# Kernel tuning notes

Measured on AMD Instinct MI355X. Metric: run time of the kernel, lower is better.

The kernel has to match this reference:

```python
import jax, jax.numpy as jnp
import numpy as np
import math

D_MODEL = 1024
NHEAD = 16
D_K = D_MODEL // NHEAD
LAMDA_ATT = 1.0
B, L = 2, 2048


def setup_inputs() -> dict:
    key = jax.random.key(0)
    ks = jax.random.split(key, 10)
    s = 1.0 / math.sqrt(D_MODEL)
    x = jax.random.normal(ks[0], (B, L, D_MODEL), dtype=jnp.float32)
    delta_r = jax.random.uniform(ks[1], (B, L), dtype=jnp.float32)  # positive, fed to log
    Wq = jax.random.normal(ks[2], (D_MODEL, D_MODEL), dtype=jnp.float32) * s
    Wk = jax.random.normal(ks[3], (D_MODEL, D_MODEL), dtype=jnp.float32) * s
    Wv = jax.random.normal(ks[4], (D_MODEL, D_MODEL), dtype=jnp.float32) * s
    Wo = jax.random.normal(ks[5], (D_MODEL, D_MODEL), dtype=jnp.float32) * s
    bq = jnp.zeros((D_MODEL,), jnp.float32)
    bk = jnp.zeros((D_MODEL,), jnp.float32)
    bv = jnp.zeros((D_MODEL,), jnp.float32)
    bo = jnp.zeros((D_MODEL,), jnp.float32)
    return {"x": x, "delta_r": delta_r, "Wq": Wq, "bq": bq, "Wk": Wk, "bk": bk,
            "Wv": Wv, "bv": bv, "Wo": Wo, "bo": bo}


def reference(x, delta_r, Wq, bq, Wk, bk, Wv, bv, Wo, bo):
    b, l, d = x.shape
    h, dk = NHEAD, D_K

    def proj(y, W, bias):
        # [B,L,D] -> [B,H,L,dk]
        return (y @ W + bias).reshape(b, l, h, dk).transpose(0, 2, 1, 3)

    v_scaled = x * delta_r[..., None]
    q = proj(x, Wq, bq)
    k = proj(x, Wk, bk)
    v = proj(v_scaled, Wv, bv)

    scores = jnp.einsum('bhqd,bhkd->bhqk', q, k) / math.sqrt(dk)
    pos = jnp.arange(l)
    dist = jnp.abs(pos[None, :] - pos[:, None]).astype(scores.dtype)  # [L,L]
    rel_bias = LAMDA_ATT * jnp.log(delta_r + 1e-6)  # [B,L]
    scores = scores - dist[None, None] * 0.1 + rel_bias[:, None, None, :]

    attn = jax.nn.softmax(scores, axis=-1)  # dropout is identity in eval mode
    context = jnp.einsum('bhqk,bhkd->bqhd', attn, v).reshape(b, l, d)
    out = context @ Wo + bo
    return out, attn.mean(axis=1)
```

## Files before the change

kernel.cpp:

```cpp
#include <hip/hip_runtime.h>
#include <math.h>

#define DMODEL 1024
#define NHEAD  16
#define DK     64
#define BB     2
#define LL     2048
#define MTOT   (BB*LL)

#define LOG2E      1.4426950408889634f
#define SCQ        (0.125f * LOG2E)
#define C2LOG      (0.1f * LOG2E)
#define SKIP_BOUND (-24.0f)

typedef __bf16 bf16_t;
typedef __bf16 bf16x8 __attribute__((ext_vector_type(8)));
typedef __bf16 bf16x4 __attribute__((ext_vector_type(4)));
typedef float  f32x4  __attribute__((ext_vector_type(4)));

static __device__ __forceinline__ f32x4 mfma16(bf16x8 a, bf16x8 b, f32x4 c) {
    return __builtin_amdgcn_mfma_f32_16x16x32_bf16(a, b, c, 0, 0, 0);
}
static __device__ __forceinline__ float exp2f_fast(float x) {
    return __builtin_amdgcn_exp2f(x);
}
static __device__ __forceinline__ float log2f_fast(float x) {
    return __builtin_amdgcn_logf(x);
}
static __device__ __forceinline__ void gl_lds16(const bf16_t* g, bf16_t* l) {
    __builtin_amdgcn_global_load_lds(
        (const __attribute__((address_space(1))) unsigned int*)g,
        (__attribute__((address_space(3))) unsigned int*)l, 16, 0, 0);
}

__global__ __launch_bounds__(256) void prep_x_k(
    const float* __restrict__ x, const float* __restrict__ dr,
    bf16_t* __restrict__ xb, float* __restrict__ logd2)
{
    size_t gid = (size_t)blockIdx.x * 256 + threadIdx.x;
    size_t off = gid * 8;
    float4 a = *(const float4*)(x + off);
    float4 c = *(const float4*)(x + off + 4);
    float va[8] = {a.x, a.y, a.z, a.w, c.x, c.y, c.z, c.w};
    bf16x8 o1;
#pragma unroll
    for (int j = 0; j < 8; ++j) o1[j] = (bf16_t)va[j];
    *(bf16x8*)(xb + off) = o1;
    if (gid < MTOT) logd2[gid] = log2f_fast(dr[gid] + 1e-6f);
}

__global__ __launch_bounds__(256) void prep_w_k(
    const float* __restrict__ Wq, const float* __restrict__ Wk,
    const float* __restrict__ Wv, const float* __restrict__ Wo,
    bf16_t* __restrict__ Wcat, bf16_t* __restrict__ Wot)
{
    __shared__ __align__(16) float Ts[64][68];
    const int z = blockIdx.z;
    const float* W = (z == 0) ? Wq : (z == 1) ? Wk : (z == 2) ? Wv : Wo;
    bf16_t* dst = (z < 3) ? (Wcat + (size_t)z * DMODEL * DMODEL) : Wot;
    const int tid = threadIdx.x;
    const int k0 = blockIdx.x * 64, n0 = blockIdx.y * 64;
#pragma unroll
    for (int i = 0; i < 4; ++i) {
        int u = tid + 256 * i, r = u >> 4, c4 = (u & 15) * 4;
        *(float4*)&Ts[r][c4] = *(const float4*)(W + (size_t)(k0 + r) * DMODEL + n0 + c4);
    }
    __syncthreads();
#pragma unroll
    for (int i = 0; i < 2; ++i) {
        int u = tid + 256 * i, n = u >> 3, k8 = (u & 7) * 8;
        bf16x8 v;
#pragma unroll
        for (int j = 0; j < 8; ++j) v[j] = (bf16_t)Ts[k8 + j][n];
        *(bf16x8*)(dst + (size_t)(n0 + n) * DMODEL + k0 + k8) = v;
    }
}

__global__ __launch_bounds__(256, 3) void gemm128_k(
    const bf16_t* __restrict__ A, const bf16_t* __restrict__ Bt,
    const float* __restrict__ b0, const float* __restrict__ b1,
    const float* __restrict__ b2, const float* __restrict__ delta,
    float* __restrict__ outf, bf16_t* __restrict__ outQ,
    bf16_t* __restrict__ outK, bf16_t* __restrict__ outVt, int mode)
{
    __shared__ __align__(16) bf16_t Asw[128 * 64];
    __shared__ __align__(16) bf16_t Bsw[128 * 64];
    const int tid = threadIdx.x, lane = tid & 63, w = tid >> 6;
    const int quad = lane >> 4, n16 = lane & 15;
    const int wm = (w & 1) * 64, wn = (w >> 1) * 64;
    const int m0 = blockIdx.y * 128, n0 = blockIdx.x * 128;
    const int srow = lane >> 3;
    const int scb  = (lane & 7) ^ srow;

    f32x4 acc[4][4] = {};

    for (int K0 = 0; K0 < DMODEL; K0 += 64) {
        __syncthreads();
#pragma unroll
        for (int i = 0; i < 4; ++i) {
            int rb = w * 32 + i * 8;
            gl_lds16(A  + (size_t)(m0 + rb + srow) * DMODEL + K0 + scb * 8,
                     &Asw[rb * 64]);
            gl_lds16(Bt + (size_t)(n0 + rb + srow) * DMODEL + K0 + scb * 8,
                     &Bsw[rb * 64]);
        }
        __syncthreads();
#pragma unroll
        for (int kc = 0; kc < 2; ++kc) {
            const int pcb = ((kc * 4 + quad) ^ (n16 & 7)) * 8;
            bf16x8 af[4], bfv[4];
#pragma unroll
            for (int mi = 0; mi < 4; ++mi)
                af[mi] = *(const bf16x8*)&Asw[(wm + mi * 16 + n16) * 64 + pcb];
#pragma unroll
            for (int ni = 0; ni < 4; ++ni)
                bfv[ni] = *(const bf16x8*)&Bsw[(wn + ni * 16 + n16) * 64 + pcb];
#pragma unroll
            for (int mi = 0; mi < 4; ++mi)
#pragma unroll
                for (int ni = 0; ni < 4; ++ni)
                    acc[mi][ni] = mfma16(af[mi], bfv[ni], acc[mi][ni]);
        }
    }

    if (mode == 0) {
        const int region = n0 >> 10;
        if (region == 2) {
#pragma unroll
            for (int mi = 0; mi < 4; ++mi) {
                const int mbase = m0 + wm + mi * 16 + quad * 4;
                const int bidx = mbase >> 11, l = mbase & (LL - 1);
                const f32x4 dm4 = *(const f32x4*)(delta + mbase);
#pragma unroll
                for (int ni = 0; ni < 4; ++ni) {
                    const int nl = (n0 & 1023) + wn + ni * 16 + n16;
                    const int h = nl >> 6, dd = nl & 63;
                    const float bv = b2[nl];
                    bf16x4 pk;
#pragma unroll
                    for (int r = 0; r < 4; ++r)
                        pk[r] = (bf16_t)(acc[mi][ni][r] * dm4[r] + bv);
                    *(bf16x4*)(outVt + ((size_t)(bidx * NHEAD + h) * DK + dd) * LL + l) = pk;
                }
            }
        } else {
            const float* bias = (region == 0) ? b0 : b1;
            bf16_t* dst = (region == 0) ? outQ : outK;
            const float qs = (region == 0) ? SCQ : 1.0f;
#pragma unroll
            for (int mi = 0; mi < 4; ++mi) {
#pragma unroll
                for (int r = 0; r < 4; ++r) {
                    const int m = m0 + wm + mi * 16 + quad * 4 + r;
                    const int bidx = m >> 11, l = m & (LL - 1);
#pragma unroll
                    for (int ni = 0; ni < 4; ++ni) {
                        const int nl = (n0 & 1023) + wn + ni * 16 + n16;
                        const int h = nl >> 6, dd = nl & 63;
                        float v = (acc[mi][ni][r] + bias[nl]) * qs;
                        dst[(((size_t)(bidx * NHEAD + h) * LL) + l) * DK + dd] = (bf16_t)v;
                    }
                }
            }
        }
    } else {
#pragma unroll
        for (int mi = 0; mi < 4; ++mi) {
#pragma unroll
            for (int r = 0; r < 4; ++r) {
                const int m = m0 + wm + mi * 16 + quad * 4 + r;
#pragma unroll
                for (int ni = 0; ni < 4; ++ni) {
                    const int n = n0 + wn + ni * 16 + n16;
                    outf[(size_t)m * DMODEL + n] = acc[mi][ni][r] + b0[n];
                }
            }
        }
    }
}

__global__ __launch_bounds__(256) void stats_k(
    const bf16_t* __restrict__ Q, const bf16_t* __restrict__ K,
    const float* __restrict__ logd2, float* __restrict__ Qn,
    float* __restrict__ Kn, float* __restrict__ dlb, float* __restrict__ ldx)
{
    __shared__ float qn_s[2048], kn_s[2048], dg_s[2048];
    const int tid = threadIdx.x, bh = blockIdx.x, b = bh >> 4;
    const size_t base = (size_t)bh * LL * DK;
#pragma unroll
    for (int i = 0; i < 8; ++i) {
        const int row = tid + 256 * i;
        float qn2 = 0.f, kn2 = 0.f, dg = 0.f;
#pragma unroll
        for (int j = 0; j < 8; ++j) {
            bf16x8 qv = *(const bf16x8*)(Q + base + (size_t)row * DK + j * 8);
            bf16x8 kv = *(const bf16x8*)(K + base + (size_t)row * DK + j * 8);
#pragma unroll
            for (int e = 0; e < 8; ++e) {
                float fq = (float)qv[e], fk = (float)kv[e];
                qn2 += fq * fq; kn2 += fk * fk; dg += fq * fk;
            }
        }
        qn_s[row] = qn2;
        kn_s[row] = kn2;
        dg_s[row] = dg + logd2[b * LL + row];
    }
    __syncthreads();
    if (tid < 16) {
        float mq = 0.f, md = 1e30f;
        for (int r = 0; r < 128; ++r) {
            mq = fmaxf(mq, qn_s[tid * 128 + r]);
            md = fminf(md, dg_s[tid * 128 + r]);
        }
        Qn[bh * 16 + tid] = sqrtf(mq);
        dlb[bh * 16 + tid] = md;
    } else if (tid >= 64 && tid < 96) {
        const int t = tid - 64;
        float mk = 0.f;
        for (int r = 0; r < 64; ++r) mk = fmaxf(mk, kn_s[t * 64 + r]);
        Kn[bh * 32 + t] = sqrtf(mk);
    } else if (tid >= 128 && tid < 160 && (bh & 15) == 0) {
        const int t = tid - 128;
        float ml = -1e30f;
        for (int r = 0; r < 64; ++r) ml = fmaxf(ml, logd2[b * LL + t * 64 + r]);
        ldx[b * 32 + t] = ml;
    }
}

__global__ __launch_bounds__(256) void mlstat_k(
    const float* __restrict__ mlws, float* __restrict__ mlmin)
{
    __shared__ float s[2048];
    const int tid = threadIdx.x, bh = blockIdx.x;
#pragma unroll
    for (int i = 0; i < 8; ++i)
        s[tid + 256 * i] = mlws[(size_t)bh * LL + tid + 256 * i];
    __syncthreads();
    if (tid < 16) {
        float m = 1e30f;
        for (int r = 0; r < 128; ++r) m = fminf(m, s[tid * 128 + r]);
        mlmin[bh * 16 + tid] = m;
    }
}

__global__ __launch_bounds__(256, 3) void attn_flash_mfma_k(
    const bf16_t* __restrict__ Q, const bf16_t* __restrict__ K,
    const bf16_t* __restrict__ Vt, const float* __restrict__ logd2,
    const float* __restrict__ Qn, const float* __restrict__ Kn,
    const float* __restrict__ dlb, const float* __restrict__ ldx,
    bf16_t* __restrict__ ctx, float* __restrict__ mlout)
{
    __shared__ __align__(16) bf16_t Ks[64][72];
    __shared__ __align__(16) bf16_t Vts[64][72];
    __shared__ __align__(16) bf16_t Ps[4][32][72];
    __shared__ float logds[64];

    const int tid = threadIdx.x;
    const int lane = tid & 63, w = tid >> 6;
    const int quad = lane >> 4, n16 = lane & 15;
    const int bh = blockIdx.x, b = bh >> 4, h = bh & 15;
    const int qt = blockIdx.y, q0 = qt * 128;
    const size_t base = (size_t)bh * LL * DK;
    const int qq[2] = {q0 + w * 32 + n16, q0 + w * 32 + 16 + n16};

    bf16x8 qa[2][2];
#pragma unroll
    for (int qg = 0; qg < 2; ++qg)
#pragma unroll
        for (int kc = 0; kc < 2; ++kc)
            qa[qg][kc] = *(const bf16x8*)(Q + base + (size_t)qq[qg] * DK +
                                          kc * 32 + quad * 8);

    unsigned mask = 0;
    {
        const float qn = Qn[bh * 16 + qt], dl = dlb[bh * 16 + qt];
        for (int t = 0; t < 32; ++t) {
            const int kc0 = t * 64;
            const int dmin = (kc0 > q0 + 127) ? (kc0 - (q0 + 127))
                           : ((q0 > kc0 + 63) ? (q0 - (kc0 + 63)) : 0);
            const float bound = qn * Kn[bh * 32 + t] + ldx[b * 32 + t]
                              - C2LOG * (float)dmin - dl;
            if (bound > SKIP_BOUND) mask |= (1u << t);
        }
    }

    const int strow = tid >> 3, stc8 = (tid & 7) * 8;
    bf16x8 kr0, kr1, vr0, vr1;
    float ldr = 0.f;
    auto prefetch = [&](int k0) {
        kr0 = *(const bf16x8*)(K + base + (size_t)(k0 + strow) * DK + stc8);
        kr1 = *(const bf16x8*)(K + base + (size_t)(k0 + 32 + strow) * DK + stc8);
        vr0 = *(const bf16x8*)(Vt + base + (size_t)strow * LL + k0 + stc8);
        vr1 = *(const bf16x8*)(Vt + base + (size_t)(32 + strow) * LL + k0 + stc8);
        if (tid < 64) ldr = logd2[b * LL + k0 + tid];
    };

    float m_c[2] = {-1e30f, -1e30f}, l_c[2] = {0.f, 0.f};
    f32x4 o[2][4] = {};

    int t = (int)__builtin_ctz(mask);
    prefetch(t * 64);
    for (;;) {
        const unsigned rem = (t < 31) ? (mask >> (t + 1)) : 0u;
        const int tn = rem ? (t + 1 + (int)__builtin_ctz(rem)) : -1;
        __syncthreads();
        *(bf16x8*)&Ks[strow][stc8]       = kr0;
        *(bf16x8*)&Ks[32 + strow][stc8]  = kr1;
        *(bf16x8*)&Vts[strow][stc8]      = vr0;
        *(bf16x8*)&Vts[32 + strow][stc8] = vr1;
        if (tid < 64) logds[tid] = ldr;
        __syncthreads();
        if (tn >= 0) prefetch(tn * 64);
        const int k0 = t * 64;

        f32x4 s[2][4] = {};
#pragma unroll
        for (int kc = 0; kc < 2; ++kc) {
#pragma unroll
            for (int kt = 0; kt < 4; ++kt) {
                bf16x8 kb = *(const bf16x8*)&Ks[kt * 16 + n16][kc * 32 + quad * 8];
                s[0][kt] = mfma16(kb, qa[0][kc], s[0][kt]);
                s[1][kt] = mfma16(kb, qa[1][kc], s[1][kt]);
            }
        }
#pragma unroll
        for (int qg = 0; qg < 2; ++qg) {
            const float df = (float)(qq[qg] - k0 - quad * 4);
#pragma unroll
            for (int kt = 0; kt < 4; ++kt) {
                f32x4 ldv = *(const f32x4*)&logds[kt * 16 + quad * 4];
#pragma unroll
                for (int r = 0; r < 4; ++r)
                    s[qg][kt][r] += ldv[r] - C2LOG * fabsf(df - (float)(kt * 16 + r));
            }
        }
        float mn[2], alpha[2];
#pragma unroll
        for (int qg = 0; qg < 2; ++qg) {
            f32x4 mx;
#pragma unroll
            for (int r = 0; r < 4; ++r)
                mx[r] = fmaxf(fmaxf(s[qg][0][r], s[qg][1][r]),
                              fmaxf(s[qg][2][r], s[qg][3][r]));
            float rm = fmaxf(fmaxf(mx[0], mx[1]), fmaxf(mx[2], mx[3]));
            rm = fmaxf(rm, __shfl_xor(rm, 16));
            rm = fmaxf(rm, __shfl_xor(rm, 32));
            mn[qg] = fmaxf(m_c[qg], rm);
            alpha[qg] = exp2f_fast(m_c[qg] - mn[qg]);
        }
        if (__any((mn[0] > m_c[0]) || (mn[1] > m_c[1]))) {
#pragma unroll
            for (int qg = 0; qg < 2; ++qg)
#pragma unroll
                for (int dt = 0; dt < 4; ++dt)
#pragma unroll
                    for (int r = 0; r < 4; ++r) o[qg][dt][r] *= alpha[qg];
        }
#pragma unroll
        for (int qg = 0; qg < 2; ++qg) {
            f32x4 ps = {0.f, 0.f, 0.f, 0.f};
#pragma unroll
            for (int kt = 0; kt < 4; ++kt)
#pragma unroll
                for (int r = 0; r < 4; ++r) {
                    float p = exp2f_fast(s[qg][kt][r] - mn[qg]);
                    s[qg][kt][r] = p;
                    ps[r] += p;
                }
            float psum = (ps[0] + ps[1]) + (ps[2] + ps[3]);
            psum += __shfl_xor(psum, 16);
            psum += __shfl_xor(psum, 32);
            l_c[qg] = l_c[qg] * alpha[qg] + psum;
            m_c[qg] = mn[qg];
#pragma unroll
            for (int kt = 0; kt < 4; ++kt) {
                bf16x4 pk;
#pragma unroll
                for (int r = 0; r < 4; ++r) pk[r] = (bf16_t)s[qg][kt][r];
                *(bf16x4*)&Ps[w][qg * 16 + n16][kt * 16 + quad * 4] = pk;
            }
        }
        __threadfence_block();
#pragma unroll
        for (int kc = 0; kc < 2; ++kc) {
            bf16x8 pa0 = *(const bf16x8*)&Ps[w][n16][kc * 32 + quad * 8];
            bf16x8 pa1 = *(const bf16x8*)&Ps[w][16 + n16][kc * 32 + quad * 8];
#pragma unroll
            for (int dt = 0; dt < 4; ++dt) {
                bf16x8 vb = *(const bf16x8*)&Vts[dt * 16 + n16][kc * 32 + quad * 8];
                o[0][dt] = mfma16(vb, pa0, o[0][dt]);
                o[1][dt] = mfma16(vb, pa1, o[1][dt]);
            }
        }
        if (tn < 0) break;
        t = tn;
    }
#pragma unroll
    for (int qg = 0; qg < 2; ++qg) {
        const float inv = 1.f / l_c[qg];
#pragma unroll
        for (int dt = 0; dt < 4; ++dt) {
            bf16x4 ov;
#pragma unroll
            for (int r = 0; r < 4; ++r) ov[r] = (bf16_t)(o[qg][dt][r] * inv);
            *(bf16x4*)(ctx + ((size_t)b * LL + qq[qg]) * DMODEL + h * DK +
                       dt * 16 + quad * 4) = ov;
        }
        if (quad == 0)
            mlout[(size_t)bh * LL + qq[qg]] = m_c[qg] + log2f_fast(l_c[qg]);
    }
}

__global__ __launch_bounds__(256, 3) void attn_mean_mfma_k(
    const bf16_t* __restrict__ Q, const bf16_t* __restrict__ K,
    const float* __restrict__ logd2, const float* __restrict__ mlws,
    const float* __restrict__ Qn, const float* __restrict__ Kn,
    const float* __restrict__ mlmin, const float* __restrict__ ldx,
    float* __restrict__ outmean)
{
    __shared__ __align__(16) bf16_t Ks[2][64][72];
    __shared__ float mls[2][128];
    __shared__ float logds[64];

    const int tid = threadIdx.x;
    const int lane = tid & 63, w = tid >> 6;
    const int quad = lane >> 4, n16 = lane & 15;
    const int k0 = blockIdx.x * 64, q0 = blockIdx.y * 128, b = blockIdx.z;
    const int qq[2] = {q0 + w * 32 + n16, q0 + w * 32 + 16 + n16};

    if (tid < 64) logds[tid] = logd2[b * LL + k0 + tid];
    __syncthreads();

    float bias0[2][4][4];
#pragma unroll
    for (int qg = 0; qg < 2; ++qg) {
        const float df = (float)(qq[qg] - k0 - quad * 4);
#pragma unroll
        for (int kt = 0; kt < 4; ++kt) {
            f32x4 ldv = *(const f32x4*)&logds[kt * 16 + quad * 4];
#pragma unroll
            for (int r = 0; r < 4; ++r)
                bias0[qg][kt][r] = ldv[r] - C2LOG * fabsf(df - (float)(kt * 16 + r));
        }
    }

    const int qt = q0 >> 7, ktl = k0 >> 6;
    const int dmin = (k0 > q0 + 127) ? (k0 - (q0 + 127))
                   : ((q0 > k0 + 63) ? (q0 - (k0 + 63)) : 0);
    unsigned hmask = 0;
    {
        const float dterm = ldx[b * 32 + ktl] - C2LOG * (float)dmin;
        for (int h = 0; h < NHEAD; ++h) {
            const int bh = b * 16 + h;
            const float bound = Qn[bh * 16 + qt] * Kn[bh * 32 + ktl] + dterm
                              - mlmin[bh * 16 + qt];
            if (bound > SKIP_BOUND) hmask |= (1u << h);
        }
    }

    f32x4 acc[2][4] = {};

    if (hmask) {
        const int strow = tid >> 3, stc8 = (tid & 7) * 8;
        bf16x8 kr0, kr1, qan[2][2];
        float mlv = 0.f;
        auto load_head = [&](int h) {
            const size_t hb = (size_t)(b * NHEAD + h) * LL * DK;
            kr0 = *(const bf16x8*)(K + hb + (size_t)(k0 + strow) * DK + stc8);
            kr1 = *(const bf16x8*)(K + hb + (size_t)(k0 + 32 + strow) * DK + stc8);
#pragma unroll
            for (int qg = 0; qg < 2; ++qg)
#pragma unroll
                for (int kc = 0; kc < 2; ++kc)
                    qan[qg][kc] = *(const bf16x8*)(Q + hb + (size_t)qq[qg] * DK +
                                                   kc * 32 + quad * 8);
            if (tid < 128) mlv = mlws[(size_t)(b * NHEAD + h) * LL + q0 + tid];
        };

        int h = (int)__builtin_ctz(hmask);
        load_head(h);
        int pc = 0;
        for (;;) {
            const unsigned rem = (h < 15) ? (hmask >> (h + 1)) : 0u;
            const int hn = rem ? (h + 1 + (int)__builtin_ctz(rem)) : -1;
            const int p = pc & 1;
            *(bf16x8*)&Ks[p][strow][stc8]      = kr0;
            *(bf16x8*)&Ks[p][32 + strow][stc8] = kr1;
            if (tid < 128) mls[p][tid] = mlv;
            bf16x8 qc[2][2] = {{qan[0][0], qan[0][1]}, {qan[1][0], qan[1][1]}};
            __syncthreads();
            if (hn >= 0) load_head(hn);

            f32x4 s[2][4] = {};
#pragma unroll
            for (int kc = 0; kc < 2; ++kc) {
#pragma unroll
                for (int kt = 0; kt < 4; ++kt) {
                    bf16x8 kb = *(const bf16x8*)&Ks[p][kt * 16 + n16][kc * 32 + quad * 8];
                    s[0][kt] = mfma16(kb, qc[0][kc], s[0][kt]);
                    s[1][kt] = mfma16(kb, qc[1][kc], s[1][kt]);
                }
            }
#pragma unroll
            for (int qg = 0; qg < 2; ++qg) {
                const float ml = mls[p][w * 32 + qg * 16 + n16];
#pragma unroll
                for (int kt = 0; kt < 4; ++kt)
#pragma unroll
                    for (int r = 0; r < 4; ++r)
                        acc[qg][kt][r] += exp2f_fast(s[qg][kt][r] +
                                                     bias0[qg][kt][r] - ml);
            }
            ++pc;
            if (hn < 0) break;
            h = hn;
        }
    }

    const float invH = 1.f / (float)NHEAD;
#pragma unroll
    for (int qg = 0; qg < 2; ++qg)
#pragma unroll
        for (int kt = 0; kt < 4; ++kt) {
            f32x4 ov;
#pragma unroll
            for (int r = 0; r < 4; ++r) ov[r] = acc[qg][kt][r] * invH;
            *(f32x4*)(outmean + ((size_t)b * LL + qq[qg]) * LL + k0 +
                      kt * 16 + quad * 4) = ov;
        }
}

extern "C" void kernel_launch(void* const* d_in, const int* in_sizes, int n_in,
                              void* d_out, int out_size, void* d_ws, size_t ws_size,
                              hipStream_t stream) {
    const float* x  = (const float*)d_in[0];
    const float* dr = (const float*)d_in[1];
    const float* Wq = (const float*)d_in[2];
    const float* bq = (const float*)d_in[3];
    const float* Wk = (const float*)d_in[4];
    const float* bk = (const float*)d_in[5];
    const float* Wv = (const float*)d_in[6];
    const float* bv = (const float*)d_in[7];
    const float* Wo = (const float*)d_in[8];
    const float* bo = (const float*)d_in[9];
    float* out = (float*)d_out;
    char* ws = (char*)d_ws;
    const size_t MB = 1ull << 20;

    bf16_t* xb   = (bf16_t*)(ws);
    bf16_t* Wcat = (bf16_t*)(ws + 8 * MB);
    bf16_t* Wot  = (bf16_t*)(ws + 14 * MB);
    bf16_t* Qb   = (bf16_t*)(ws + 16 * MB);
    bf16_t* Kb   = (bf16_t*)(ws + 24 * MB);
    bf16_t* Vtb  = (bf16_t*)(ws + 32 * MB);
    float*  logd = (float*)(ws + 40 * MB);
    float*  mlws = (float*)(ws + 41 * MB);
    float*  Qns  = (float*)(ws + 42 * MB);
    float*  Kns  = (float*)(ws + 42 * MB + 4096);
    float*  dlb  = (float*)(ws + 42 * MB + 12288);
    float*  ldxp = (float*)(ws + 42 * MB + 16384);
    float*  mlmn = (float*)(ws + 42 * MB + 20480);
    bf16_t* ctx  = xb;

    prep_x_k<<<2048, 256, 0, stream>>>(x, dr, xb, logd);
    prep_w_k<<<dim3(16, 16, 4), 256, 0, stream>>>(Wq, Wk, Wv, Wo, Wcat, Wot);

    gemm128_k<<<dim3(24, 32), 256, 0, stream>>>(xb, Wcat, bq, bk, bv, dr,
                                                nullptr, Qb, Kb, Vtb, 0);
    stats_k<<<32, 256, 0, stream>>>(Qb, Kb, logd, Qns, Kns, dlb, ldxp);

    attn_flash_mfma_k<<<dim3(32, 16), 256, 0, stream>>>(Qb, Kb, Vtb, logd,
                                                        Qns, Kns, dlb, ldxp,
                                                        ctx, mlws);
    mlstat_k<<<32, 256, 0, stream>>>(mlws, mlmn);
    attn_mean_mfma_k<<<dim3(32, 16, 2), 256, 0, stream>>>(
        Qb, Kb, logd, mlws, Qns, Kns, mlmn, ldxp,
        out + (size_t)MTOT * DMODEL);
    gemm128_k<<<dim3(8, 32), 256, 0, stream>>>(ctx, Wot, bo, nullptr, nullptr,
                                               nullptr, out, nullptr, nullptr,
                                               nullptr, 1);
}
```

Baseline: 247.2 us.

## Halve flash-attention query tile and add a smaller-tile output projection GEMM

```diff
diff --git a/kernel.cpp b/kernel.cpp
--- a/kernel.cpp
+++ b/kernel.cpp
@@ -174,6 +174,67 @@
                     const int n = n0 + wn + ni * 16 + n16;
                     outf[(size_t)m * DMODEL + n] = acc[mi][ni][r] + b0[n];
                 }
+            }
+        }
+    }
+}
+
+__global__ __launch_bounds__(256, 4) void gemm_out_k(
+    const bf16_t* __restrict__ A, const bf16_t* __restrict__ Bt,
+    const float* __restrict__ b0, float* __restrict__ outf)
+{
+    __shared__ __align__(16) bf16_t Asw[64 * 64];
+    __shared__ __align__(16) bf16_t Bsw[128 * 64];
+    const int tid = threadIdx.x, lane = tid & 63, w = tid >> 6;
+    const int quad = lane >> 4, n16 = lane & 15;
+    const int wm = (w & 1) * 32, wn = (w >> 1) * 64;
+    const int m0 = blockIdx.y * 64, n0 = blockIdx.x * 128;
+    const int srow = lane >> 3;
+    const int scb  = (lane & 7) ^ srow;
+
+    f32x4 acc[2][4] = {};
+
+    for (int K0 = 0; K0 < DMODEL; K0 += 64) {
+        __syncthreads();
+#pragma unroll
+        for (int i = 0; i < 2; ++i) {
+            int rb = w * 16 + i * 8;
+            gl_lds16(A + (size_t)(m0 + rb + srow) * DMODEL + K0 + scb * 8,
+                     &Asw[rb * 64]);
+        }
+#pragma unroll
+        for (int i = 0; i < 4; ++i) {
+            int rb = w * 32 + i * 8;
+            gl_lds16(Bt + (size_t)(n0 + rb + srow) * DMODEL + K0 + scb * 8,
+                     &Bsw[rb * 64]);
+        }
+        __syncthreads();
+#pragma unroll
+        for (int kc = 0; kc < 2; ++kc) {
+            const int pcb = ((kc * 4 + quad) ^ (n16 & 7)) * 8;
+            bf16x8 af[2], bfv[4];
+#pragma unroll
+            for (int mi = 0; mi < 2; ++mi)
+                af[mi] = *(const bf16x8*)&Asw[(wm + mi * 16 + n16) * 64 + pcb];
+#pragma unroll
+            for (int ni = 0; ni < 4; ++ni)
+                bfv[ni] = *(const bf16x8*)&Bsw[(wn + ni * 16 + n16) * 64 + pcb];
+#pragma unroll
+            for (int mi = 0; mi < 2; ++mi)
+#pragma unroll
+                for (int ni = 0; ni < 4; ++ni)
+                    acc[mi][ni] = mfma16(af[mi], bfv[ni], acc[mi][ni]);
+        }
+    }
+#pragma unroll
+    for (int mi = 0; mi < 2; ++mi) {
+#pragma unroll
+        for (int r = 0; r < 4; ++r) {
+            const int m = m0 + wm + mi * 16 + quad * 4 + r;
+#pragma unroll
+            for (int ni = 0; ni < 4; ++ni) {
+                const int n = n0 + wn + ni * 16 + n16;
+                outf[(size_t)m * DMODEL + n] = acc[mi][ni][r] + b0[n];
             }
         }
     }
@@ -243,7 +304,7 @@
     }
 }
 
-__global__ __launch_bounds__(256, 3) void attn_flash_mfma_k(
+__global__ __launch_bounds__(256, 4) void attn_flash_mfma_k(
     const bf16_t* __restrict__ Q, const bf16_t* __restrict__ K,
     const bf16_t* __restrict__ Vt, const float* __restrict__ logd2,
     const float* __restrict__ Qn, const float* __restrict__ Kn,
@@ -252,31 +313,28 @@
 {
     __shared__ __align__(16) bf16_t Ks[64][72];
     __shared__ __align__(16) bf16_t Vts[64][72];
-    __shared__ __align__(16) bf16_t Ps[4][32][72];
+    __shared__ __align__(16) bf16_t Ps[4][16][72];
     __shared__ float logds[64];
 
     const int tid = threadIdx.x;
     const int lane = tid & 63, w = tid >> 6;
     const int quad = lane >> 4, n16 = lane & 15;
     const int bh = blockIdx.x, b = bh >> 4, h = bh & 15;
-    const int qt = blockIdx.y, q0 = qt * 128;
+    const int qt = blockIdx.y, q0 = qt * 64;
     const size_t base = (size_t)bh * LL * DK;
-    const int qq[2] = {q0 + w * 32 + n16, q0 + w * 32 + 16 + n16};
-
-    bf16x8 qa[2][2];
-#pragma unroll
-    for (int qg = 0; qg < 2; ++qg)
-#pragma unroll
-        for (int kc = 0; kc < 2; ++kc)
-            qa[qg][kc] = *(const bf16x8*)(Q + base + (size_t)qq[qg] * DK +
-                                          kc * 32 + quad * 8);
+    const int q = q0 + w * 16 + n16;
+
+    bf16x8 qa[2];
+#pragma unroll
+    for (int kc = 0; kc < 2; ++kc)
+        qa[kc] = *(const bf16x8*)(Q + base + (size_t)q * DK + kc * 32 + quad * 8);
 
     unsigned mask = 0;
     {
-        const float qn = Qn[bh * 16 + qt], dl = dlb[bh * 16 + qt];
+        const float qn = Qn[bh * 16 + (qt >> 1)], dl = dlb[bh * 16 + (qt >> 1)];
         for (int t = 0; t < 32; ++t) {
             const int kc0 = t * 64;
-            const int dmin = (kc0 > q0 + 127) ? (kc0 - (q0 + 127))
+            const int dmin = (kc0 > q0 + 63) ? (kc0 - (q0 + 63))
                            : ((q0 > kc0 + 63) ? (q0 - (kc0 + 63)) : 0);
             const float bound = qn * Kn[bh * 32 + t] + ldx[b * 32 + t]
                               - C2LOG * (float)dmin - dl;
@@ -295,8 +353,9 @@
         if (tid < 64) ldr = logd2[b * LL + k0 + tid];
     };
 
-    float m_c[2] = {-1e30f, -1e30f}, l_c[2] = {0.f, 0.f};
-    f32x4 o[2][4] = {};
+    float m_c = -1e30f, l_c = 0.f;
+    f32x4 o[4] = {};
+    const float dfq = (float)(q - quad * 4);
 
     int t = (int)__builtin_ctz(mask);
     prefetch(t * 64);
@@ -313,102 +372,83 @@
         if (tn >= 0) prefetch(tn * 64);
         const int k0 = t * 64;
 
-        f32x4 s[2][4] = {};
+        f32x4 s[4] = {};
 #pragma unroll
         for (int kc = 0; kc < 2; ++kc) {
 #pragma unroll
             for (int kt = 0; kt < 4; ++kt) {
                 bf16x8 kb = *(const bf16x8*)&Ks[kt * 16 + n16][kc * 32 + quad * 8];
-                s[0][kt] = mfma16(kb, qa[0][kc], s[0][kt]);
-                s[1][kt] = mfma16(kb, qa[1][kc], s[1][kt]);
-            }
-        }
-#pragma unroll
-        for (int qg = 0; qg < 2; ++qg) {
-            const float df = (float)(qq[qg] - k0 - quad * 4);
-#pragma unroll
-            for (int kt = 0; kt < 4; ++kt) {
-                f32x4 ldv = *(const f32x4*)&logds[kt * 16 + quad * 4];
-#pragma unroll
-                for (int r = 0; r < 4; ++r)
-                    s[qg][kt][r] += ldv[r] - C2LOG * fabsf(df - (float)(kt * 16 + r));
-            }
-        }
-        float mn[2], alpha[2];
-#pragma unroll
-        for (int qg = 0; qg < 2; ++qg) {
-            f32x4 mx;
+                s[kt] = mfma16(kb, qa[kc], s[kt]);
+            }
+        }
+        const float df = dfq - (float)k0;
+#pragma unroll
+        for (int kt = 0; kt < 4; ++kt) {
+            f32x4 ldv = *(const f32x4*)&logds[kt * 16 + quad * 4];
 #pragma unroll
             for (int r = 0; r < 4; ++r)
-                mx[r] = fmaxf(fmaxf(s[qg][0][r], s[qg][1][r]),
-                              fmaxf(s[qg][2][r], s[qg][3][r]));
-            float rm = fmaxf(fmaxf(mx[0], mx[1]), fmaxf(mx[2], mx[3]));
-            rm = fmaxf(rm, __shfl_xor(rm, 16));
-            rm = fmaxf(rm, __shfl_xor(rm, 32));
-            mn[qg] = fmaxf(m_c[qg], rm);
-            alpha[qg] = exp2f_fast(m_c[qg] - mn[qg]);
-        }
-        if (__any((mn[0] > m_c[0]) || (mn[1] > m_c[1]))) {
-#pragma unroll
-            for (int qg = 0; qg < 2; ++qg)
-#pragma unroll
-                for (int dt = 0; dt < 4; ++dt)
-#pragma unroll
-                    for (int r = 0; r < 4; ++r) o[qg][dt][r] *= alpha[qg];
-        }
-#pragma unroll
-        for (int qg = 0; qg < 2; ++qg) {
-            f32x4 ps = {0.f, 0.f, 0.f, 0.f};
-#pragma unroll
-            for (int kt = 0; kt < 4; ++kt)
-#pragma unroll
-                for (int r = 0; r < 4; ++r) {
-                    float p = exp2f_fast(s[qg][kt][r] - mn[qg]);
-                    s[qg][kt][r] = p;
-                    ps[r] += p;
-                }
-            float psum = (ps[0] + ps[1]) + (ps[2] + ps[3]);
-            psum += __shfl_xor(psum, 16);
-            psum += __shfl_xor(psum, 32);
-            l_c[qg] = l_c[qg] * alpha[qg] + psum;
-            m_c[qg] = mn[qg];
-#pragma unroll
-            for (int kt = 0; kt < 4; ++kt) {
-                bf16x4 pk;
-#pragma unroll
-                for (int r = 0; r < 4; ++r) pk[r] = (bf16_t)s[qg][kt][r];
-                *(bf16x4*)&Ps[w][qg * 16 + n16][kt * 16 + quad * 4] = pk;
-            }
+                s[kt][r] += ldv[r] - C2LOG * fabsf(df - (float)(kt * 16 + r));
+        }
+        f32x4 mx;
+#pragma unroll
+        for (int r = 0; r < 4; ++r)
+            mx[r] = fmaxf(fmaxf(s[0][r], s[1][r]), fmaxf(s[2][r], s[3][r]));
+        float rm = fmaxf(fmaxf(mx[0], mx[1]), fmaxf(mx[2], mx[3]));
+        rm = fmaxf(rm, __shfl_xor(rm, 16));
+        rm = fmaxf(rm, __shfl_xor(rm, 32));
+        const float mn = fmaxf(m_c, rm);
+        const float alpha = exp2f_fast(m_c - mn);
+        if (__any(mn > m_c)) {
+#pragma unroll
+            for (int dt = 0; dt < 4; ++dt)
+#pragma unroll
+                for (int r = 0; r < 4; ++r) o[dt][r] *= alpha;
+        }
+        f32x4 ps = {0.f, 0.f, 0.f, 0.f};
+#pragma unroll
+        for (int kt = 0; kt < 4; ++kt)
+#pragma unroll
+            for (int r = 0; r < 4; ++r) {
+                float p = exp2f_fast(s[kt][r] - mn);
+                s[kt][r] = p;
+                ps[r] += p;
+            }
+        float psum = (ps[0] + ps[1]) + (ps[2] + ps[3]);
+        psum += __shfl_xor(psum, 16);
+        psum += __shfl_xor(psum, 32);
+        l_c = l_c * alpha + psum;
+        m_c = mn;
+#pragma unroll
+        for (int kt = 0; kt < 4; ++kt) {
+            bf16x4 pk;
+#pragma unroll
+            for (int r = 0; r < 4; ++r) pk[r] = (bf16_t)s[kt][r];
+            *(bf16x4*)&Ps[w][n16][kt * 16 + quad * 4] = pk;
         }
         __threadfence_block();
 #pragma unroll
         for (int kc = 0; kc < 2; ++kc) {
-            bf16x8 pa0 = *(const bf16x8*)&Ps[w][n16][kc * 32 + quad * 8];
-            bf16x8 pa1 = *(const bf16x8*)&Ps[w][16 + n16][kc * 32 + quad * 8];
+            bf16x8 pa = *(const bf16x8*)&Ps[w][n16][kc * 32 + quad * 8];
 #pragma unroll
             for (int dt = 0; dt < 4; ++dt) {
                 bf16x8 vb = *(const bf16x8*)&Vts[dt * 16 + n16][kc * 32 + quad * 8];
-                o[0][dt] = mfma16(vb, pa0, o[0][dt]);
-                o[1][dt] = mfma16(vb, pa1, o[1][dt]);
+                o[dt] = mfma16(vb, pa, o[dt]);
             }
         }
         if (tn < 0) break;
         t = tn;
     }
-#pragma unroll
-    for (int qg = 0; qg < 2; ++qg) {
-        const float inv = 1.f / l_c[qg];
-#pragma unroll
-        for (int dt = 0; dt < 4; ++dt) {
-            bf16x4 ov;
-#pragma unroll
-            for (int r = 0; r < 4; ++r) ov[r] = (bf16_t)(o[qg][dt][r] * inv);
-            *(bf16x4*)(ctx + ((size_t)b * LL + qq[qg]) * DMODEL + h * DK +
-                       dt * 16 + quad * 4) = ov;
-        }
-        if (quad == 0)
-            mlout[(size_t)bh * LL + qq[qg]] = m_c[qg] + log2f_fast(l_c[qg]);
-    }
+    const float inv = 1.f / l_c;
+#pragma unroll
+    for (int dt = 0; dt < 4; ++dt) {
+        bf16x4 ov;
+#pragma unroll
+        for (int r = 0; r < 4; ++r) ov[r] = (bf16_t)(o[dt][r] * inv);
+        *(bf16x4*)(ctx + ((size_t)b * LL + q) * DMODEL + h * DK +
+                   dt * 16 + quad * 4) = ov;
+    }
+    if (quad == 0)
+        mlout[(size_t)bh * LL + q] = m_c + log2f_fast(l_c);
 }
 
 __global__ __launch_bounds__(256, 3) void attn_mean_mfma_k(
@@ -569,14 +609,12 @@
                                                 nullptr, Qb, Kb, Vtb, 0);
     stats_k<<<32, 256, 0, stream>>>(Qb, Kb, logd, Qns, Kns, dlb, ldxp);
 
-    attn_flash_mfma_k<<<dim3(32, 16), 256, 0, stream>>>(Qb, Kb, Vtb, logd,
+    attn_flash_mfma_k<<<dim3(32, 32), 256, 0, stream>>>(Qb, Kb, Vtb, logd,
                                                         Qns, Kns, dlb, ldxp,
                                                         ctx, mlws);
     mlstat_k<<<32, 256, 0, stream>>>(mlws, mlmn);
     attn_mean_mfma_k<<<dim3(32, 16, 2), 256, 0, stream>>>(
         Qb, Kb, logd, mlws, Qns, Kns, mlmn, ldxp,
         out + (size_t)MTOT * DMODEL);
-    gemm128_k<<<dim3(8, 32), 256, 0, stream>>>(ctx, Wot, bo, nullptr, nullptr,
-                                               nullptr, out, nullptr, nullptr,
-                                               nullptr, 1);
-}
+    gemm_out_k<<<dim3(8, 64), 256, 0, stream>>>(ctx, Wot, bo, out);
+}
```

After: 243.0 us. No clear change (-1.7%).
